# Kernel optimization log

Measured on AMD Instinct MI355X. Metric: run time of the kernel, lower is better.

The kernel has to match this reference:

```python
import jax, jax.numpy as jnp
import numpy as np

# Sampled-neighborhood cascade sizes (src->dst per layer) and edge counts
N0, N1, N2, N3 = 400000, 200000, 100000, 50000
E1, E2, E3 = 500000, 300000, 150000
DIN, DH = 128, 128


def setup_inputs() -> dict:
    key = jax.random.key(0)
    ks = jax.random.split(key, 24)
    inp = {}
    inp['x'] = jax.random.normal(ks[0], (N0, DIN), jnp.float32)
    inp['src1'] = jax.random.randint(ks[1], (E1,), 0, N0, dtype=jnp.int64)
    inp['dst1'] = jax.random.randint(ks[2], (E1,), 0, N1, dtype=jnp.int64)
    inp['src2'] = jax.random.randint(ks[3], (E2,), 0, N1, dtype=jnp.int64)
    inp['dst2'] = jax.random.randint(ks[4], (E2,), 0, N2, dtype=jnp.int64)
    inp['src3'] = jax.random.randint(ks[5], (E3,), 0, N2, dtype=jnp.int64)
    inp['dst3'] = jax.random.randint(ks[6], (E3,), 0, N3, dtype=jnp.int64)
    # SAGEConv params: lin_l (on aggregated neighbors, with bias), lin_r (root, no bias)
    dims = [(DIN, DH), (DH, DH), (DH, DH)]
    for i, (di, do) in enumerate(dims, start=1):
        s = 1.0 / np.sqrt(di)
        inp[f'Wl{i}'] = jax.random.uniform(ks[6 + 4 * i - 3], (di, do), jnp.float32, -s, s)
        inp[f'Wr{i}'] = jax.random.uniform(ks[6 + 4 * i - 2], (di, do), jnp.float32, -s, s)
        inp[f'b{i}'] = jax.random.uniform(ks[6 + 4 * i - 1], (do,), jnp.float32, -s, s)
        inp[f'a{i}'] = jnp.full((do,), 0.25, jnp.float32)  # PReLU per-channel init
    return inp


def _sage_prelu(x_src, n_dst, src, dst, Wl, Wr, b, alpha):
    # mean aggregation over incoming edges (PyG SAGEConv default aggr='mean')
    x_dst = x_src[:n_dst]                                   # [n_dst, d]
    msg = x_src[src]                                        # [E, d] gather
    summed = jax.ops.segment_sum(msg, dst, num_segments=n_dst)
    cnt = jax.ops.segment_sum(jnp.ones(src.shape[0], x_src.dtype), dst,
                              num_segments=n_dst)
    mean = summed / jnp.maximum(cnt, 1.0)[:, None]
    out = mean @ Wl + b + x_dst @ Wr                        # lin_l(aggr) + lin_r(root)
    return jnp.where(out > 0, out, alpha * out)             # per-channel PReLU


def reference(x, src1, dst1, src2, dst2, src3, dst3,
              Wl1, Wr1, b1, a1, Wl2, Wr2, b2, a2, Wl3, Wr3, b3, a3):
    h = _sage_prelu(x, N1, src1, dst1, Wl1, Wr1, b1, a1)
    h = _sage_prelu(h, N2, src2, dst2, Wl2, Wr2, b2, a2)
    h = _sage_prelu(h, N3, src3, dst3, Wl3, Wr3, b3, a3)
    return h  # [N3, DH]
```

## Files before the change

### kernel.cpp

```cpp
#include <hip/hip_runtime.h>


constexpr int cN0 = 400000, cN1 = 200000, cN2 = 100000, cN3 = 50000;
constexpr int cE1 = 500000, cE2 = 300000, cE3 = 150000;
constexpr int cNT = cN1 + cN2 + cN3;
constexpr int cET = cE1 + cE2 + cE3;

#define NDIV_UP(a, b) (((a) + (b) - 1) / (b))

typedef __attribute__((ext_vector_type(8))) short bf16x8;
typedef __attribute__((ext_vector_type(4))) float f32x4;
typedef __attribute__((ext_vector_type(4))) unsigned u32x4;

__device__ __forceinline__ unsigned fbits(float f) {
  return __builtin_bit_cast(unsigned, f);
}
__device__ __forceinline__ float ffrom(unsigned u) {
  return __builtin_bit_cast(float, u);
}
__device__ __forceinline__ unsigned short f2bf(float f) {
  unsigned u = fbits(f);
  unsigned r = u + 0x7FFFu + ((u >> 16) & 1u);
  return (unsigned short)(r >> 16);
}

__global__ void detect_idx64_kernel(const long long* __restrict__ p, int E,
                                    long long nmax, int* __restrict__ flag) {
  int t = threadIdx.x;
  int n = E < 512 ? E : 512;
  int bad = 0;
  for (int i = t; i < n; i += 64) {
    long long v = p[i];
    if (v < 0 || v >= nmax) bad = 1;
  }
  unsigned long long b = __ballot(bad);
  if (t == 0) *flag = (b == 0ull) ? 1 : 0;
}

__device__ __forceinline__ int load_idx(const void* p, int i, int flag) {
  return flag ? (int)((const long long*)p)[i] : ((const int*)p)[i];
}

__global__ void hist3_kernel(const void* __restrict__ d1, const void* __restrict__ d2,
                             const void* __restrict__ d3, const int* __restrict__ flag,
                             int* __restrict__ CNT) {
  int e = blockIdx.x * 256 + threadIdx.x;
  if (e >= cET) return;
  int f = *flag;
  int d;
  if (e < cE1) d = load_idx(d1, e, f);
  else if (e < cE1 + cE2) d = cN1 + load_idx(d2, e - cE1, f);
  else d = cN1 + cN2 + load_idx(d3, e - cE1 - cE2, f);
  atomicAdd(&CNT[d], 1);
}

__global__ __launch_bounds__(256) void scan_reduce(const int* __restrict__ cnt,
                                                   int n, int* __restrict__ bsum) {
  __shared__ int s[256];
  int t = threadIdx.x;
  int base = blockIdx.x * 1024 + t * 4;
  int v = 0;
  if (base + 3 < n) {
    int4 c = *(const int4*)(cnt + base);
    v = c.x + c.y + c.z + c.w;
  } else {
    for (int i = 0; i < 4; ++i)
      if (base + i < n) v += cnt[base + i];
  }
  s[t] = v;
  __syncthreads();
  for (int off = 128; off > 0; off >>= 1) {
    if (t < off) s[t] += s[t + off];
    __syncthreads();
  }
  if (t == 0) bsum[blockIdx.x] = s[0];
}

__global__ __launch_bounds__(256) void scan_bsums(int* __restrict__ bsum, int nb) {
  __shared__ int s[256];
  int t = threadIdx.x;
  int v0 = (2 * t < nb) ? bsum[2 * t] : 0;
  int v1 = (2 * t + 1 < nb) ? bsum[2 * t + 1] : 0;
  int p = v0 + v1;
  s[t] = p;
  __syncthreads();
  for (int off = 1; off < 256; off <<= 1) {
    int x = (t >= off) ? s[t - off] : 0;
    __syncthreads();
    s[t] += x;
    __syncthreads();
  }
  int excl = s[t] - p;
  if (2 * t < nb) bsum[2 * t] = excl;
  if (2 * t + 1 < nb) bsum[2 * t + 1] = excl + v0;
}

__global__ __launch_bounds__(256) void scan_final(const int* __restrict__ cnt,
                                                  int n, const int* __restrict__ bsum,
                                                  int* __restrict__ offs) {
  __shared__ int s[256];
  int t = threadIdx.x;
  int base = blockIdx.x * 1024 + t * 4;
  int v0 = 0, v1 = 0, v2 = 0, v3 = 0;
  if (base + 3 < n) {
    int4 c = *(const int4*)(cnt + base);
    v0 = c.x; v1 = c.y; v2 = c.z; v3 = c.w;
  } else {
    if (base + 0 < n) v0 = cnt[base + 0];
    if (base + 1 < n) v1 = cnt[base + 1];
    if (base + 2 < n) v2 = cnt[base + 2];
  }
  int tsum = v0 + v1 + v2 + v3;
  s[t] = tsum;
  __syncthreads();
  for (int off = 1; off < 256; off <<= 1) {
    int x = (t >= off) ? s[t - off] : 0;
    __syncthreads();
    s[t] += x;
    __syncthreads();
  }
  int excl = s[t] - tsum;
  int o = bsum[blockIdx.x] + excl;
  if (base + 0 < n) offs[base + 0] = o;
  o += v0;
  if (base + 1 < n) offs[base + 1] = o;
  o += v1;
  if (base + 2 < n) offs[base + 2] = o;
  o += v2;
  if (base + 3 < n) offs[base + 3] = o;
}

__global__ void fill3_kernel(const void* __restrict__ s1, const void* __restrict__ d1,
                             const void* __restrict__ s2, const void* __restrict__ d2,
                             const void* __restrict__ s3, const void* __restrict__ d3,
                             const int* __restrict__ flag,
                             int* __restrict__ OFFS, int* __restrict__ EID) {
  int e = blockIdx.x * 256 + threadIdx.x;
  if (e >= cET) return;
  int f = *flag;
  int s, d;
  if (e < cE1) {
    s = load_idx(s1, e, f);
    d = load_idx(d1, e, f);
  } else if (e < cE1 + cE2) {
    int i = e - cE1;
    s = load_idx(s2, i, f);
    d = cN1 + load_idx(d2, i, f);
  } else {
    int i = e - cE1 - cE2;
    s = load_idx(s3, i, f);
    d = cN1 + cN2 + load_idx(d3, i, f);
  }
  int pos = atomicAdd(&OFFS[d], 1);
  EID[pos] = s;
}

__global__ void pack_w3_kernel(const float* __restrict__ Wl1, const float* __restrict__ Wr1,
                               const float* __restrict__ Wl2, const float* __restrict__ Wr2,
                               const float* __restrict__ Wl3, const float* __restrict__ Wr3,
                               unsigned short* __restrict__ wpk) {
  int idx = blockIdx.x * 256 + threadIdx.x;
  if (idx >= 3 * 16384) return;
  int L = idx >> 14;
  int r = idx & 16383;
  const float* Wl = L == 0 ? Wl1 : (L == 1 ? Wl2 : Wl3);
  const float* Wr = L == 0 ? Wr1 : (L == 1 ? Wr2 : Wr3);
  unsigned short* o = wpk + L * 32768;
  int j = r & 7, l = (r >> 3) & 63, cf = (r >> 9) & 7, ks = r >> 12;
  int k = ks * 32 + (l >> 4) * 8 + j;
  int col = cf * 16 + (l & 15);
  o[r] = f2bf(Wl[k * 128 + col]);
  o[16384 + r] = f2bf(Wr[k * 128 + col]);
}

template <bool SRCF32>
__global__ __launch_bounds__(256) void gather_kernel(
    const void* __restrict__ hsrc, const int* __restrict__ OFFS,
    const int* __restrict__ EID, int rowoff,
    unsigned short* __restrict__ meanB, int n) {
  int row = blockIdx.x * 4 + (threadIdx.x >> 6);
  if (row >= n) return;
  int lane = threadIdx.x & 63;
  int gr = rowoff + row;
  int start = gr ? OFFS[gr - 1] : 0;
  int end = OFFS[gr];
  float a0 = 0.f, a1 = 0.f, b0 = 0.f, b1 = 0.f;
  int i = start;
  for (; i + 1 < end; i += 2) {
    int s0 = EID[i], s1 = EID[i + 1];
    if (SRCF32) {
      float2 v0 = *(const float2*)((const float*)hsrc + (size_t)s0 * 128 + lane * 2);
      float2 v1 = *(const float2*)((const float*)hsrc + (size_t)s1 * 128 + lane * 2);
      a0 += v0.x; a1 += v0.y;
      b0 += v1.x; b1 += v1.y;
    } else {
      unsigned u0 = *(const unsigned*)((const unsigned short*)hsrc + (size_t)s0 * 128 + lane * 2);
      unsigned u1 = *(const unsigned*)((const unsigned short*)hsrc + (size_t)s1 * 128 + lane * 2);
      a0 += ffrom(u0 << 16); a1 += ffrom(u0 & 0xFFFF0000u);
      b0 += ffrom(u1 << 16); b1 += ffrom(u1 & 0xFFFF0000u);
    }
  }
  if (i < end) {
    int s0 = EID[i];
    if (SRCF32) {
      float2 v0 = *(const float2*)((const float*)hsrc + (size_t)s0 * 128 + lane * 2);
      a0 += v0.x; a1 += v0.y;
    } else {
      unsigned u0 = *(const unsigned*)((const unsigned short*)hsrc + (size_t)s0 * 128 + lane * 2);
      a0 += ffrom(u0 << 16); a1 += ffrom(u0 & 0xFFFF0000u);
    }
  }
  a0 += b0; a1 += b1;
  float inv = (end > start) ? 1.0f / (float)(end - start) : 0.0f;
  unsigned o = (unsigned)f2bf(a0 * inv) | ((unsigned)f2bf(a1 * inv) << 16);
  *(unsigned*)(meanB + (size_t)row * 128 + lane * 2) = o;
}

template <bool XF32, bool OUTF32>
__global__ __launch_bounds__(256) void gemm_kernel(
    const unsigned short* __restrict__ meanB, const void* __restrict__ xsrc,
    const unsigned short* __restrict__ W,
    const float* __restrict__ bias, const float* __restrict__ alpha,
    void* __restrict__ outp, int n) {
  const int lane = threadIdx.x & 63;
  const int wv = threadIdx.x >> 6;
  const int rbase = blockIdx.x * 128 + wv * 32;
  const int g = lane >> 4;
  const int r16 = lane & 15;

  f32x4 acc[2][8] = {};

  for (int ks = 0; ks < 4; ++ks) {
    bf16x8 am[2], ax[2];
#pragma unroll
    for (int t = 0; t < 2; ++t) {
      const int row = rbase + t * 16 + r16;
      if (row < n) {
        am[t] = *(const bf16x8*)(meanB + (size_t)row * 128 + ks * 32 + g * 8);
        if (XF32) {
          const float* xp = (const float*)xsrc + (size_t)row * 128 + ks * 32 + g * 8;
          float xv[8];
          *(float4*)&xv[0] = *(const float4*)(xp);
          *(float4*)&xv[4] = *(const float4*)(xp + 4);
          u32x4 w;
#pragma unroll
          for (int p = 0; p < 4; ++p) {
            w[p] = (unsigned)f2bf(xv[2 * p]) | ((unsigned)f2bf(xv[2 * p + 1]) << 16);
          }
          ax[t] = __builtin_bit_cast(bf16x8, w);
        } else {
          ax[t] = *(const bf16x8*)((const unsigned short*)xsrc + (size_t)row * 128 + ks * 32 + g * 8);
        }
      } else {
        am[t] = (bf16x8)0;
        ax[t] = (bf16x8)0;
      }
    }
    const unsigned short* wb = W + (size_t)ks * 4096 + (size_t)lane * 8;
#pragma unroll
    for (int cf = 0; cf < 8; ++cf) {
      const unsigned short* wp = wb + cf * 512;
      bf16x8 wl = *(const bf16x8*)(wp);
      bf16x8 wr = *(const bf16x8*)(wp + 16384);
#pragma unroll
      for (int t = 0; t < 2; ++t) {
        acc[t][cf] = __builtin_amdgcn_mfma_f32_16x16x32_bf16(am[t], wl, acc[t][cf], 0, 0, 0);
        acc[t][cf] = __builtin_amdgcn_mfma_f32_16x16x32_bf16(ax[t], wr, acc[t][cf], 0, 0, 0);
      }
    }
  }

  const int ocol0 = lane & 15;
  const int orow_off = (lane >> 4) * 4;
#pragma unroll
  for (int cf = 0; cf < 8; ++cf) {
    const int ocol = cf * 16 + ocol0;
    const float b = bias[ocol];
    const float a = alpha[ocol];
#pragma unroll
    for (int t = 0; t < 2; ++t) {
      const int orb = rbase + t * 16 + orow_off;
#pragma unroll
      for (int i = 0; i < 4; ++i) {
        const int orow = orb + i;
        if (orow < n) {
          float v = acc[t][cf][i] + b;
          v = v > 0.f ? v : a * v;
          if (OUTF32) {
            ((float*)outp)[(size_t)orow * 128 + ocol] = v;
          } else {
            ((unsigned short*)outp)[(size_t)orow * 128 + ocol] = f2bf(v);
          }
        }
      }
    }
  }
}

extern "C" void kernel_launch(void* const* d_in, const int* in_sizes, int n_in,
                              void* d_out, int out_size, void* d_ws, size_t ws_size,
                              hipStream_t stream) {
  const float* x = (const float*)d_in[0];
  const void* src1 = d_in[1];
  const void* dst1 = d_in[2];
  const void* src2 = d_in[3];
  const void* dst2 = d_in[4];
  const void* src3 = d_in[5];
  const void* dst3 = d_in[6];
  const float* Wl1 = (const float*)d_in[7];
  const float* Wr1 = (const float*)d_in[8];
  const float* b1  = (const float*)d_in[9];
  const float* a1  = (const float*)d_in[10];
  const float* Wl2 = (const float*)d_in[11];
  const float* Wr2 = (const float*)d_in[12];
  const float* b2  = (const float*)d_in[13];
  const float* a2  = (const float*)d_in[14];
  const float* Wl3 = (const float*)d_in[15];
  const float* Wr3 = (const float*)d_in[16];
  const float* b3  = (const float*)d_in[17];
  const float* a3  = (const float*)d_in[18];

  unsigned short* M1 = (unsigned short*)d_ws;
  unsigned short* M2 = M1 + (size_t)cN1 * 128;
  unsigned short* M3 = M2 + (size_t)cN2 * 128;
  int* CNT = (int*)(M3 + (size_t)cN3 * 128);
  int* OFFS = CNT + cNT;
  int* EID = OFFS + cNT;
  int* bsum = EID + cET;
  int* flag = bsum + 1024;
  unsigned short* wpk = (unsigned short*)(flag + 64);

  const int nb = NDIV_UP(cNT, 1024);

  detect_idx64_kernel<<<1, 64, 0, stream>>>((const long long*)src1, cE1,
                                            (long long)cN0, flag);
  pack_w3_kernel<<<192, 256, 0, stream>>>(Wl1, Wr1, Wl2, Wr2, Wl3, Wr3, wpk);
  hipMemsetAsync(CNT, 0, (size_t)cNT * sizeof(int), stream);
  hist3_kernel<<<NDIV_UP(cET, 256), 256, 0, stream>>>(dst1, dst2, dst3, flag, CNT);
  scan_reduce<<<nb, 256, 0, stream>>>(CNT, cNT, bsum);
  scan_bsums<<<1, 256, 0, stream>>>(bsum, nb);
  scan_final<<<nb, 256, 0, stream>>>(CNT, cNT, bsum, OFFS);
  fill3_kernel<<<NDIV_UP(cET, 256), 256, 0, stream>>>(src1, dst1, src2, dst2,
                                                      src3, dst3, flag, OFFS, EID);

  gather_kernel<true><<<NDIV_UP(cN1, 4), 256, 0, stream>>>(
      x, OFFS, EID, 0, M1, cN1);
  gemm_kernel<true, false><<<NDIV_UP(cN1, 128), 256, 0, stream>>>(
      M1, x, wpk, b1, a1, M1, cN1);

  gather_kernel<false><<<NDIV_UP(cN2, 4), 256, 0, stream>>>(
      M1, OFFS, EID, cN1, M2, cN2);
  gemm_kernel<false, false><<<NDIV_UP(cN2, 128), 256, 0, stream>>>(
      M2, M1, wpk + 32768, b2, a2, M2, cN2);

  gather_kernel<false><<<NDIV_UP(cN3, 4), 256, 0, stream>>>(
      M2, OFFS, EID, cN1 + cN2, M3, cN3);
  gemm_kernel<false, true><<<NDIV_UP(cN3, 128), 256, 0, stream>>>(
      M3, M2, wpk + 65536, b3, a3, d_out, cN3);
}
```

Before: 397.5 us.

## Stage GEMM weights in LDS and prefetch all activation rows up front

The GEMM kernel now copies the whole packed bf16 weight matrix (Wl and Wr, 64 KB) into shared memory once per block and reads MFMA operands from LDS rather than global memory. All activation and root-feature loads for the four k-steps are issued before the weight copy and barrier, so their latency overlaps the LDS fill. The fp32-to-bf16 conversion moves after the barrier. This raises register and LDS use per block (launch bounds now ask for 2 blocks per SM), which may limit occupancy, and it adds a 64 KB global-to-LDS copy to every block.

```diff
diff --git a/kernel.cpp b/kernel.cpp
--- a/kernel.cpp
+++ b/kernel.cpp
@@ -217,46 +217,76 @@
 }
 
 template <bool XF32, bool OUTF32>
-__global__ __launch_bounds__(256) void gemm_kernel(
+__global__ __launch_bounds__(256, 2) void gemm_kernel(
     const unsigned short* __restrict__ meanB, const void* __restrict__ xsrc,
     const unsigned short* __restrict__ W,
     const float* __restrict__ bias, const float* __restrict__ alpha,
     void* __restrict__ outp, int n) {
-  const int lane = threadIdx.x & 63;
-  const int wv = threadIdx.x >> 6;
+  __shared__ __align__(16) unsigned short wlds[32768];
+  const int tid = threadIdx.x;
+  const int lane = tid & 63;
+  const int wv = tid >> 6;
   const int rbase = blockIdx.x * 128 + wv * 32;
   const int g = lane >> 4;
   const int r16 = lane & 15;
 
-  f32x4 acc[2][8] = {};
-
-  for (int ks = 0; ks < 4; ++ks) {
-    bf16x8 am[2], ax[2];
-#pragma unroll
-    for (int t = 0; t < 2; ++t) {
-      const int row = rbase + t * 16 + r16;
-      if (row < n) {
-        am[t] = *(const bf16x8*)(meanB + (size_t)row * 128 + ks * 32 + g * 8);
+  bf16x8 am[2][4], ax[2][4];
+  float4 xr[2][4][2];
+#pragma unroll
+  for (int t = 0; t < 2; ++t) {
+    const int row = rbase + t * 16 + r16;
+    const bool ok = row < n;
+#pragma unroll
+    for (int ks = 0; ks < 4; ++ks) {
+      if (ok) {
+        am[t][ks] = *(const bf16x8*)(meanB + (size_t)row * 128 + ks * 32 + g * 8);
         if (XF32) {
           const float* xp = (const float*)xsrc + (size_t)row * 128 + ks * 32 + g * 8;
-          float xv[8];
-          *(float4*)&xv[0] = *(const float4*)(xp);
-          *(float4*)&xv[4] = *(const float4*)(xp + 4);
-          u32x4 w;
-#pragma unroll
-          for (int p = 0; p < 4; ++p) {
-            w[p] = (unsigned)f2bf(xv[2 * p]) | ((unsigned)f2bf(xv[2 * p + 1]) << 16);
-          }
-          ax[t] = __builtin_bit_cast(bf16x8, w);
+          xr[t][ks][0] = *(const float4*)(xp);
+          xr[t][ks][1] = *(const float4*)(xp + 4);
         } else {
-          ax[t] = *(const bf16x8*)((const unsigned short*)xsrc + (size_t)row * 128 + ks * 32 + g * 8);
+          ax[t][ks] = *(const bf16x8*)((const unsigned short*)xsrc +
+                                       (size_t)row * 128 + ks * 32 + g * 8);
         }
       } else {
-        am[t] = (bf16x8)0;
-        ax[t] = (bf16x8)0;
+        am[t][ks] = (bf16x8)0;
+        if (XF32) {
+          xr[t][ks][0] = make_float4(0.f, 0.f, 0.f, 0.f);
+          xr[t][ks][1] = make_float4(0.f, 0.f, 0.f, 0.f);
+        } else {
+          ax[t][ks] = (bf16x8)0;
+        }
       }
     }
-    const unsigned short* wb = W + (size_t)ks * 4096 + (size_t)lane * 8;
+  }
+
+  {
+    const float4* Wg = (const float4*)W;
+    float4* Ws = (float4*)wlds;
+#pragma unroll
+    for (int i = 0; i < 16; ++i)
+      Ws[i * 256 + tid] = Wg[i * 256 + tid];
+  }
+  __syncthreads();
+
+  if (XF32) {
+#pragma unroll
+    for (int t = 0; t < 2; ++t)
+#pragma unroll
+      for (int ks = 0; ks < 4; ++ks) {
+        const float* xv = (const float*)&xr[t][ks][0];
+        u32x4 w;
+#pragma unroll
+        for (int p = 0; p < 4; ++p)
+          w[p] = (unsigned)f2bf(xv[2 * p]) | ((unsigned)f2bf(xv[2 * p + 1]) << 16);
+        ax[t][ks] = __builtin_bit_cast(bf16x8, w);
+      }
+  }
+
+  f32x4 acc[2][8] = {};
+#pragma unroll
+  for (int ks = 0; ks < 4; ++ks) {
+    const unsigned short* wb = wlds + ks * 4096 + lane * 8;
 #pragma unroll
     for (int cf = 0; cf < 8; ++cf) {
       const unsigned short* wp = wb + cf * 512;
@@ -264,8 +294,8 @@
       bf16x8 wr = *(const bf16x8*)(wp + 16384);
 #pragma unroll
       for (int t = 0; t < 2; ++t) {
-        acc[t][cf] = __builtin_amdgcn_mfma_f32_16x16x32_bf16(am[t], wl, acc[t][cf], 0, 0, 0);
-        acc[t][cf] = __builtin_amdgcn_mfma_f32_16x16x32_bf16(ax[t], wr, acc[t][cf], 0, 0, 0);
+        acc[t][cf] = __builtin_amdgcn_mfma_f32_16x16x32_bf16(am[t][ks], wl, acc[t][cf], 0, 0, 0);
+        acc[t][cf] = __builtin_amdgcn_mfma_f32_16x16x32_bf16(ax[t][ks], wr, acc[t][cf], 0, 0, 0);
       }
     }
   }
```

After: 363.1 us. 8.7% less time.
